# Kernel optimization log

Measured on AMD Instinct MI355X. Metric: run time of the kernel, lower is better.

Reference implementation:

```python
import jax, jax.numpy as jnp
import numpy as np

B, S, D, H, SKG = 4, 1024, 1024, 16, 256
HD = D // H  # head dim = 64


def setup_inputs() -> dict:
    key = jax.random.key(0)
    ks = jax.random.split(key, 8)
    std = 0.02
    return {
        "x": jax.random.normal(ks[0], (B, S, D), dtype=jnp.float32),
        "pred_kg": jax.random.normal(ks[1], (B, SKG, D), dtype=jnp.float32),
        "Wc": jax.random.normal(ks[2], (D, 3 * D), dtype=jnp.float32) * std,  # c_attn weight
        "bc": jnp.zeros((3 * D,), dtype=jnp.float32),
        "Wk": jax.random.normal(ks[3], (D, 2 * D), dtype=jnp.float32) * std,  # k_attn weight
        "bk": jnp.zeros((2 * D,), dtype=jnp.float32),
        "Wp": jax.random.normal(ks[4], (D, D), dtype=jnp.float32) * std,     # c_proj weight (shared)
        "bp": jnp.zeros((D,), dtype=jnp.float32),
    }


def _split_heads(t):  # [B, T, D] -> [B, H, T, HD]
    Bb, T, _ = t.shape
    return t.reshape(Bb, T, H, HD).transpose(0, 2, 1, 3)


def _merge_heads(t):  # [B, H, T, HD] -> [B, T, D]
    Bb, _, T, _ = t.shape
    return t.transpose(0, 2, 1, 3).reshape(Bb, T, D)


def reference(x, pred_kg, Wc, bc, Wk, bk, Wp, bp):
    # ---- self-attention branch (GPT-2 style, explicit causal bias blend) ----
    qkv = x @ Wc + bc                       # Conv1D: [B,S,3D]
    q, k, v = jnp.split(qkv, 3, axis=-1)
    q = _split_heads(q)                     # [B,H,S,HD]
    k = _split_heads(k)
    v = _split_heads(v)

    inv_sqrt_d = 1.0 / jnp.sqrt(jnp.float32(HD))
    w = jnp.einsum("bhqd,bhkd->bhqk", q, k) * inv_sqrt_d  # [B,H,S,S]
    causal = jnp.tril(jnp.ones((S, S), dtype=w.dtype))    # bias buffer slice b
    # faithful to: w = w * b - 10000.0 * (1 - b)
    w = w * causal - 10000.0 * (1.0 - causal)
    w = jax.nn.softmax(w, axis=-1)
    a = jnp.einsum("bhqk,bhkd->bhqd", w, v)
    a = _merge_heads(a) @ Wp + bp           # c_proj; resid dropout is identity in eval

    # ---- KG cross-attention branch (shares query and c_proj) ----
    kkv = pred_kg @ Wk + bk                 # [B,SKG,2D]
    kk, kv = jnp.split(kkv, 2, axis=-1)
    kk = _split_heads(kk)                   # [B,H,SKG,HD]
    kv = _split_heads(kv)
    w2 = jnp.einsum("bhqd,bhkd->bhqk", q, kk) * inv_sqrt_d  # [B,H,S,SKG]
    w2 = jax.nn.softmax(w2, axis=-1)
    ka = jnp.einsum("bhqk,bhkd->bhqd", w2, kv)
    ka = _merge_heads(ka) @ Wp + bp

    # concat the two branch outputs along the sequence axis: [B, S+SKG, D]
    return jnp.concatenate([a, ka], axis=1)
```

## Files before the change

### kernel.cpp

```cpp
#include <hip/hip_runtime.h>
#include <hip/hip_bf16.h>

typedef __bf16 bf16_t;
typedef bf16_t bf16x8 __attribute__((ext_vector_type(8)));
typedef bf16_t bf16x4 __attribute__((ext_vector_type(4)));
typedef float f32x4 __attribute__((ext_vector_type(4)));
typedef float f32x16 __attribute__((ext_vector_type(16)));

#define EXP2C 0.1803368867f
#define FEXP2(x) __builtin_amdgcn_exp2f(x)

__device__ __forceinline__ void gload16(const void* g, void* l) {
  __builtin_amdgcn_global_load_lds(
      (const __attribute__((address_space(1))) void*)g,
      (__attribute__((address_space(3))) void*)l, 16, 0, 0);
}

__device__ __forceinline__ unsigned pkbf(float lo, float hi) {
  unsigned short a = __builtin_bit_cast(unsigned short, (bf16_t)lo);
  unsigned short b = __builtin_bit_cast(unsigned short, (bf16_t)hi);
  return (unsigned)a | ((unsigned)b << 16);
}

__device__ __forceinline__ void plswap(unsigned& a, unsigned& b) {
#if __has_builtin(__builtin_amdgcn_permlane32_swap)
  auto r = __builtin_amdgcn_permlane32_swap(a, b, false, false);
  a = r[0]; b = r[1];
#else
  asm("v_permlane32_swap_b32 %0, %1" : "+v"(a), "+v"(b));
#endif
}
__device__ __forceinline__ float xmax32(float x) {
  unsigned a = __builtin_bit_cast(unsigned, x), b = a;
  plswap(a, b);
  return fmaxf(__builtin_bit_cast(float, a), __builtin_bit_cast(float, b));
}
__device__ __forceinline__ float xsum32(float x) {
  unsigned a = __builtin_bit_cast(unsigned, x), b = a;
  plswap(a, b);
  return __builtin_bit_cast(float, a) + __builtin_bit_cast(float, b);
}

__global__ __launch_bounds__(256) void prep_kernel(
    const float* __restrict__ x, bf16_t* __restrict__ xb,
    const float* __restrict__ pkg, bf16_t* __restrict__ pkb,
    const float* __restrict__ Wc, bf16_t* __restrict__ Wct,
    const float* __restrict__ Wk, bf16_t* __restrict__ Wkt,
    const float* __restrict__ Wp, bf16_t* __restrict__ Wpt) {
  __shared__ float tile[32][33];
  const int bid = blockIdx.x, tid = threadIdx.x;
  if (bid < 5120) {
    int i = bid * 256 + tid;
    const float* src; bf16_t* dst;
    if (i < 1048576) { src = x; dst = xb; }
    else { i -= 1048576; src = pkg; dst = pkb; }
    float4 v = reinterpret_cast<const float4*>(src)[i];
    bf16x4 o = { (bf16_t)v.x, (bf16_t)v.y, (bf16_t)v.z, (bf16_t)v.w };
    reinterpret_cast<bf16x4*>(dst)[i] = o;
    return;
  }
  int r = bid - 5120;
  int xx = r % 192, ky = r / 192;
  const float* W; bf16_t* T; int N;
  if (xx < 96) { W = Wc; T = Wct; N = 3072; }
  else if (xx < 160) { W = Wk; T = Wkt; N = 2048; xx -= 96; }
  else { W = Wp; T = Wpt; N = 1024; xx -= 160; }
  const int K = 1024;
  int tx = tid & 31, ty = tid >> 5;
  int n0 = xx * 32, k0 = ky * 32;
#pragma unroll
  for (int i = 0; i < 4; ++i)
    tile[ty + i * 8][tx] = W[(size_t)(k0 + ty + i * 8) * N + n0 + tx];
  __syncthreads();
#pragma unroll
  for (int i = 0; i < 4; ++i)
    T[(size_t)(n0 + ty + i * 8) * K + k0 + tx] = (bf16_t)tile[tx][ty + i * 8];
}

__global__ __launch_bounds__(256) void pack2_kernel(
    const bf16_t* __restrict__ src0, bf16_t* __restrict__ kd0, bf16_t* __restrict__ vd0,
    const bf16_t* __restrict__ src1, bf16_t* __restrict__ kd1, bf16_t* __restrict__ vd1) {
  __shared__ bf16_t vt[32][72];
  const int tid = threadIdx.x;
  int x = blockIdx.x;
  const int bh = blockIdx.y;
  const bf16_t* src; bf16_t *kd, *vd; int R, stride, kcol, vcol, NT, t;
  if (x < 32) { src = src0; kd = kd0; vd = vd0; R = 1024; stride = 3072; kcol = 1024; vcol = 2048; NT = 32; t = x; }
  else        { src = src1; kd = kd1; vd = vd1; R = 256;  stride = 2048; kcol = 0;    vcol = 1024; NT = 8;  t = x - 32; }
  const int b = bh >> 4, h = bh & 15;
  const size_t srow = (size_t)b * R + t * 32;
  const size_t obase = ((size_t)bh * NT + t) * 2048;
  {
    int r = tid >> 3, c = tid & 7;
    bf16x8 d = *(const bf16x8*)&src[(srow + r) * stride + vcol + h * 64 + c * 8];
    *(bf16x8*)&vt[r][c * 8] = d;
  }
  {
    int ks = tid >> 6, l = tid & 63;
    int hi8 = (l >> 5) * 8;
    bf16x8 d = *(const bf16x8*)&src[(srow + (l & 31)) * stride + kcol + h * 64 + ks * 16 + hi8];
    *(bf16x8*)&kd[obase + ks * 512 + l * 8] = d;
  }
  __syncthreads();
  {
    int dd = tid >> 6, l = tid & 63;
    int mb = dd >> 1, ks = dd & 1;
    int hd = mb * 32 + (l & 31);
    int kvr = ks * 16 + (l >> 5) * 8;
    bf16x8 o;
#pragma unroll
    for (int j = 0; j < 8; ++j) o[j] = vt[kvr + j][hd];
    *(bf16x8*)&vd[obase + dd * 512 + l * 8] = o;
  }
}

#define GBAR() __builtin_amdgcn_s_barrier()
#define LGKM0() asm volatile("s_waitcnt lgkmcnt(0)" ::: "memory")

__device__ __forceinline__ void gemm256_body(
    char* smem, const bf16_t* __restrict__ A, const bf16_t* __restrict__ Bt,
    const float* __restrict__ bias, bf16_t* __restrict__ Cout,
    int N, int K, int bx, int by) {
  const int tid = threadIdx.x;
  const int l = tid & 63, w = tid >> 6;
  const int lr = l & 15, lg = l >> 4;
  const int m0 = by * 256, n0 = bx * 256;
  const int wr = (w >> 2) * 128, wc = (w & 3) * 64;
  const int hA = w >> 2, hB = (w >> 1) & 1;

  const int sr = tid >> 3;
  const int scb = ((tid & 7) * 16) ^ ((sr & 7) << 4);
  const bf16_t* Ab = A + (size_t)m0 * K + (scb >> 1);
  const bf16_t* Bb = Bt + (size_t)n0 * K + (scb >> 1);
  const int nk = K >> 6;
  const int xr = (lr & 7) << 4;

  auto STAGE_A = [&](int t, int h) {
    const bf16_t* g = Ab + (size_t)(h * 128 + sr) * K + t * 64;
    char* d = smem + ((size_t)(t & 1) * 2 + h) * 16384 + tid * 16;
    gload16(g, d);
    gload16(g + (size_t)64 * K, d + 8192);
  };
  auto STAGE_B = [&](int t, int h) {
    const bf16_t* g = Bb + (size_t)(h * 128 + sr) * K + t * 64;
    char* d = smem + 65536 + ((size_t)(t & 1) * 2 + h) * 16384 + tid * 16;
    gload16(g, d);
    gload16(g + (size_t)64 * K, d + 8192);
  };

  f32x4 acc[8][4] = {};
  bf16x8 af[4][2], bf[2][2][2];

  STAGE_A(0, 0); STAGE_A(0, 1); STAGE_B(0, 0); STAGE_B(0, 1);
  asm volatile("s_waitcnt vmcnt(0)" ::: "memory");
  GBAR();

  for (int t = 0; t < nk; ++t) {
    const char* pA = smem + ((size_t)(t & 1) * 2 + hA) * 16384;
    const char* pB = smem + 65536 + ((size_t)(t & 1) * 2 + hB) * 16384;
    auto LDA = [&](int mf, int ks) {
      return *(const bf16x8*)(pA + (mf * 16 + lr) * 128 + ((ks * 64 + lg * 16) ^ xr));
    };
    auto LDB = [&](int nf, int ks) {
      return *(const bf16x8*)(pB + ((w & 1) * 64 + nf * 16 + lr) * 128 + ((ks * 64 + lg * 16) ^ xr));
    };
#pragma unroll
    for (int mf = 0; mf < 4; ++mf) { af[mf][0] = LDA(mf, 0); af[mf][1] = LDA(mf, 1); }
#pragma unroll
    for (int nf = 0; nf < 2; ++nf) { bf[0][nf][0] = LDB(nf, 0); bf[0][nf][1] = LDB(nf, 1); }
    if (t + 1 < nk) { STAGE_A(t + 1, 0); STAGE_B(t + 1, 0); }
    GBAR(); LGKM0();
    __builtin_amdgcn_s_setprio(1);
#pragma unroll
    for (int mf = 0; mf < 4; ++mf)
#pragma unroll
      for (int nf = 0; nf < 2; ++nf) {
        acc[mf][nf] = __builtin_amdgcn_mfma_f32_16x16x32_bf16(af[mf][0], bf[0][nf][0], acc[mf][nf], 0, 0, 0);
        acc[mf][nf] = __builtin_amdgcn_mfma_f32_16x16x32_bf16(af[mf][1], bf[0][nf][1], acc[mf][nf], 0, 0, 0);
      }
    __builtin_amdgcn_s_setprio(0);
    GBAR();
#pragma unroll
    for (int nf = 0; nf < 2; ++nf) { bf[1][nf][0] = LDB(2 + nf, 0); bf[1][nf][1] = LDB(2 + nf, 1); }
    if (t + 1 < nk) { STAGE_A(t + 1, 1); STAGE_B(t + 1, 1); }
    GBAR(); LGKM0();
    __builtin_amdgcn_s_setprio(1);
#pragma unroll
    for (int mf = 0; mf < 4; ++mf)
#pragma unroll
      for (int nf = 0; nf < 2; ++nf) {
        acc[mf][2 + nf] = __builtin_amdgcn_mfma_f32_16x16x32_bf16(af[mf][0], bf[1][nf][0], acc[mf][2 + nf], 0, 0, 0);
        acc[mf][2 + nf] = __builtin_amdgcn_mfma_f32_16x16x32_bf16(af[mf][1], bf[1][nf][1], acc[mf][2 + nf], 0, 0, 0);
      }
    __builtin_amdgcn_s_setprio(0);
    GBAR();
#pragma unroll
    for (int mf = 0; mf < 4; ++mf) { af[mf][0] = LDA(4 + mf, 0); af[mf][1] = LDA(4 + mf, 1); }
    GBAR(); LGKM0();
    __builtin_amdgcn_s_setprio(1);
#pragma unroll
    for (int mf = 0; mf < 4; ++mf)
#pragma unroll
      for (int nf = 0; nf < 2; ++nf) {
        acc[4 + mf][nf] = __builtin_amdgcn_mfma_f32_16x16x32_bf16(af[mf][0], bf[0][nf][0], acc[4 + mf][nf], 0, 0, 0);
        acc[4 + mf][nf] = __builtin_amdgcn_mfma_f32_16x16x32_bf16(af[mf][1], bf[0][nf][1], acc[4 + mf][nf], 0, 0, 0);
      }
    __builtin_amdgcn_s_setprio(0);
    GBAR();
    __builtin_amdgcn_s_setprio(1);
#pragma unroll
    for (int mf = 0; mf < 4; ++mf)
#pragma unroll
      for (int nf = 0; nf < 2; ++nf) {
        acc[4 + mf][2 + nf] = __builtin_amdgcn_mfma_f32_16x16x32_bf16(af[mf][0], bf[1][nf][0], acc[4 + mf][2 + nf], 0, 0, 0);
        acc[4 + mf][2 + nf] = __builtin_amdgcn_mfma_f32_16x16x32_bf16(af[mf][1], bf[1][nf][1], acc[4 + mf][2 + nf], 0, 0, 0);
      }
    __builtin_amdgcn_s_setprio(0);
    asm volatile("s_waitcnt vmcnt(0)" ::: "memory");
    GBAR();
  }

#pragma unroll
  for (int mf = 0; mf < 8; ++mf) {
#pragma unroll
    for (int nf = 0; nf < 4; ++nf) {
      int col = n0 + wc + nf * 16 + lr;
      float bb = bias[col];
      int rowb = m0 + wr + mf * 16 + lg * 4;
#pragma unroll
      for (int r = 0; r < 4; ++r) {
        float v = acc[mf][nf][r] + bb;
        ((bf16_t*)Cout)[(size_t)(rowb + r) * N + col] = (bf16_t)v;
      }
    }
  }
}

__global__ __launch_bounds__(512, 1) void gemm2_kernel(
    const bf16_t* __restrict__ A0, const bf16_t* __restrict__ B0,
    const float* __restrict__ bi0, bf16_t* __restrict__ C0,
    const bf16_t* __restrict__ A1, const bf16_t* __restrict__ B1,
    const float* __restrict__ bi1, bf16_t* __restrict__ C1) {
  extern __shared__ char smem[];
  int bid = blockIdx.x;
  int wg = (bid & 7) * 28 + (bid >> 3);
  if (wg < 192)
    gemm256_body(smem, A0, B0, bi0, C0, 3072, 1024, wg % 12, wg / 12);
  else {
    int r = wg - 192;
    gemm256_body(smem, A1, B1, bi1, C1, 2048, 1024, r % 8, r / 8);
  }
}

#define MFMA2(mi, ni)                                                         \
  acc[mi][ni] = __builtin_amdgcn_mfma_f32_16x16x32_bf16(af[(mi) & 1][0], bf[ni][0], acc[mi][ni], 0, 0, 0); \
  acc[mi][ni] = __builtin_amdgcn_mfma_f32_16x16x32_bf16(af[(mi) & 1][1], bf[ni][1], acc[mi][ni], 0, 0, 0);
#define MFMA8(qm, qn)                                                         \
  MFMA2(2 * (qm) + 0, 2 * (qn) + 0) MFMA2(2 * (qm) + 0, 2 * (qn) + 1)         \
  MFMA2(2 * (qm) + 1, 2 * (qn) + 0) MFMA2(2 * (qm) + 1, 2 * (qn) + 1)

template <int OUTF32>
__device__ __forceinline__ void gemm8_body(
    char* smem, const bf16_t* __restrict__ A, const bf16_t* __restrict__ Bt,
    const float* __restrict__ bias, void* __restrict__ Cout,
    int N, int K, int bx, int by) {
  const int tid = threadIdx.x;
  const int l = tid & 63, w = tid >> 6;
  const int lr = l & 15, lg = l >> 4;
  const int m0 = by * 256, n0 = bx * 128;
  const int wr = (w >> 1) * 64, wc = (w & 1) * 64;

  const int sr = tid >> 3;
  const int scb = ((tid & 7) * 16) ^ ((sr & 7) << 4);
  const bf16_t* Ab = A + (size_t)m0 * K + (scb >> 1);
  const bf16_t* Bb = Bt + (size_t)n0 * K + (scb >> 1);
  const int nk = K >> 6;

  const int hA = w >> 2;
  const int rA = ((w >> 1) & 1) * 64 + lr;
  const int rB = wc + lr;
  const int xr = (lr & 7) << 4;

  auto STAGE_A = [&](int t, int h) {
    const bf16_t* g = Ab + (size_t)(h * 128 + sr) * K + t * 64;
    char* d = smem + ((size_t)(t & 1) * 2 + h) * 16384 + tid * 16;
    gload16(g, d);
    gload16(g + (size_t)64 * K, d + 8192);
  };
  auto STAGE_B = [&](int t) {
    const bf16_t* g = Bb + (size_t)sr * K + t * 64;
    char* d = smem + 65536 + (size_t)(t & 1) * 16384 + tid * 16;
    gload16(g, d);
    gload16(g + (size_t)64 * K, d + 8192);
  };

  f32x4 acc[4][4] = {};
  bf16x8 af[2][2], bf[4][2];

  STAGE_A(0, 0); STAGE_A(0, 1); STAGE_B(0); STAGE_B(1); STAGE_A(1, 0);
  asm volatile("s_waitcnt vmcnt(4)" ::: "memory");
  GBAR();

  for (int t = 0; t < nk; ++t) {
    const char* pA = smem + ((size_t)(t & 1) * 2 + hA) * 16384;
    const char* pB = smem + 65536 + (size_t)(t & 1) * 16384;
    auto LDA = [&](int mf, int ks) {
      return *(const bf16x8*)(pA + (rA + mf * 16) * 128 + ((ks * 64 + lg * 16) ^ xr));
    };
    auto LDB = [&](int nf, int ks) {
      return *(const bf16x8*)(pB + (rB + nf * 16) * 128 + ((ks * 64 + lg * 16) ^ xr));
    };
    af[0][0] = LDA(0, 0); af[0][1] = LDA(0, 1);
    af[1][0] = LDA(1, 0); af[1][1] = LDA(1, 1);
    bf[0][0] = LDB(0, 0); bf[0][1] = LDB(0, 1);
    bf[1][0] = LDB(1, 0); bf[1][1] = LDB(1, 1);
    if (t + 1 < nk) STAGE_A(t + 1, 1);
    GBAR(); LGKM0();
    __builtin_amdgcn_s_setprio(1);
    MFMA8(0, 0)
    __builtin_amdgcn_s_setprio(0);
    GBAR();
    bf[2][0] = LDB(2, 0); bf[2][1] = LDB(2, 1);
    bf[3][0] = LDB(3, 0); bf[3][1] = LDB(3, 1);
    GBAR(); LGKM0();
    __builtin_amdgcn_s_setprio(1);
    MFMA8(0, 1)
    __builtin_amdgcn_s_setprio(0);
    GBAR();
    af[0][0] = LDA(2, 0); af[0][1] = LDA(2, 1);
    af[1][0] = LDA(3, 0); af[1][1] = LDA(3, 1);
    if (t + 2 < nk) STAGE_B(t + 2);
    GBAR(); LGKM0();
    __builtin_amdgcn_s_setprio(1);
    MFMA8(1, 0)
    __builtin_amdgcn_s_setprio(0);
    GBAR();
    if (t + 2 < nk) STAGE_A(t + 2, 0);
    GBAR();
    __builtin_amdgcn_s_setprio(1);
    MFMA8(1, 1)
    __builtin_amdgcn_s_setprio(0);
    if (t + 2 < nk)      asm volatile("s_waitcnt vmcnt(4)" ::: "memory");
    else if (t + 1 < nk) asm volatile("s_waitcnt vmcnt(0)" ::: "memory");
    GBAR();
  }

#pragma unroll
  for (int mf = 0; mf < 4; ++mf) {
#pragma unroll
    for (int nf = 0; nf < 4; ++nf) {
      int col = n0 + wc + nf * 16 + lr;
      float bb = bias[col];
      int rowb = m0 + wr + mf * 16 + lg * 4;
#pragma unroll
      for (int r = 0; r < 4; ++r) {
        float v = acc[mf][nf][r] + bb;
        if constexpr (OUTF32)
          ((float*)Cout)[(size_t)(rowb + r) * N + col] = v;
        else
          ((bf16_t*)Cout)[(size_t)(rowb + r) * N + col] = (bf16_t)v;
      }
    }
  }
}

__global__ __launch_bounds__(512, 1) void gemm_proj_kernel(
    const bf16_t* __restrict__ A, const bf16_t* __restrict__ Bt,
    const float* __restrict__ bias, float* __restrict__ Cout) {
  extern __shared__ char smem[];
  int bid = blockIdx.x;
  int wg = (bid & 7) * 32 + (bid >> 3);
  gemm8_body<1>(smem, A, Bt, bias, Cout, 1024, 1024, wg % 8, wg / 8);
}

#define STAGE64(bf, it)                                                       \
  {                                                                           \
    gload16(kba + (size_t)(it) * 4096 + tid * 8, &sKV[bf][tid * 16]);         \
    gload16(kba + (size_t)(it) * 4096 + 2048 + tid * 8, &sKV[bf][4096 + tid * 16]); \
    gload16(vba + (size_t)(it) * 4096 + tid * 8, &sKV[bf][8192 + tid * 16]);  \
    gload16(vba + (size_t)(it) * 4096 + 2048 + tid * 8, &sKV[bf][12288 + tid * 16]); \
  }
#define QKT(sub)                                                              \
  {                                                                           \
    _Pragma("unroll") for (int c = 0; c < 4; ++c)                             \
        kf[c] = *(const bf16x8*)&sKV[buf][(sub) * 4096 + c * 1024 + l * 16];  \
    sa = (f32x16){};                                                          \
    __builtin_amdgcn_s_setprio(1);                                            \
    _Pragma("unroll") for (int ks = 0; ks < 4; ++ks)                          \
        sa = __builtin_amdgcn_mfma_f32_32x32x16_bf16(kf[ks], qf[ks], sa, 0, 0, 0); \
    __builtin_amdgcn_s_setprio(0);                                            \
  }
#define SMPV(sub, tcur)                                                       \
  {                                                                           \
    _Pragma("unroll") for (int c = 0; c < 4; ++c)                             \
        vf[c] = *(const bf16x8*)&sKV[buf][8192 + (sub) * 4096 + c * 1024 + l * 16]; \
    float sv[16];                                                             \
    const bool mt = is_self && ((tcur) == qw);                                \
    _Pragma("unroll") for (int r = 0; r < 16; ++r) {                          \
      float v = sa[r];                                                        \
      if (mt) {                                                               \
        int kvr = (r & 3) + 8 * (r >> 2) + kv4;                               \
        v = (kvr > ql) ? -1e30f : v;                                          \
      }                                                                       \
      sv[r] = v;                                                              \
    }                                                                         \
    float tm = fmaxf(                                                         \
        fmaxf(fmaxf(fmaxf(sv[0], sv[1]), fmaxf(sv[2], sv[3])),                \
              fmaxf(fmaxf(sv[4], sv[5]), fmaxf(sv[6], sv[7]))),               \
        fmaxf(fmaxf(fmaxf(sv[8], sv[9]), fmaxf(sv[10], sv[11])),              \
              fmaxf(fmaxf(sv[12], sv[13]), fmaxf(sv[14], sv[15]))));          \
    tm = xmax32(tm);                                                          \
    if (!__all(tm <= mcur + 64.f)) {                                          \
      float mn = fmaxf(mcur, tm);                                             \
      float sc = FEXP2((mcur - mn) * EXP2C);                                  \
      mcur = mn;                                                              \
      lcur *= sc;                                                             \
      _Pragma("unroll") for (int mb = 0; mb < 2; ++mb)                        \
          _Pragma("unroll") for (int r = 0; r < 16; ++r) oacc[mb][r] *= sc;   \
    }                                                                         \
    const float hm = mcur * EXP2C;                                            \
    float pf[16];                                                             \
    _Pragma("unroll") for (int r = 0; r < 16; ++r)                            \
        pf[r] = FEXP2(__builtin_fmaf(sv[r], EXP2C, -hm));                     \
    float ps = (((pf[0] + pf[1]) + (pf[2] + pf[3])) +                         \
                ((pf[4] + pf[5]) + (pf[6] + pf[7]))) +                        \
               (((pf[8] + pf[9]) + (pf[10] + pf[11])) +                       \
                ((pf[12] + pf[13]) + (pf[14] + pf[15])));                     \
    ps = xsum32(ps);                                                          \
    lcur += ps;                                                               \
    unsigned o01 = pkbf(pf[0], pf[1]), o23 = pkbf(pf[2], pf[3]);              \
    unsigned o45 = pkbf(pf[4], pf[5]), o67 = pkbf(pf[6], pf[7]);              \
    unsigned o89 = pkbf(pf[8], pf[9]), o1011 = pkbf(pf[10], pf[11]);          \
    unsigned o1213 = pkbf(pf[12], pf[13]), o1415 = pkbf(pf[14], pf[15]);      \
    plswap(o01, o45); plswap(o23, o67);                                       \
    plswap(o89, o1213); plswap(o1011, o1415);                                 \
    uint4 w0 = { o01, o23, o45, o67 };                                        \
    uint4 w1 = { o89, o1011, o1213, o1415 };                                  \
    bf16x8 pb0 = __builtin_bit_cast(bf16x8, w0);                              \
    bf16x8 pb1 = __builtin_bit_cast(bf16x8, w1);                              \
    __builtin_amdgcn_s_setprio(1);                                            \
    oacc[0] = __builtin_amdgcn_mfma_f32_32x32x16_bf16(vf[0], pb0, oacc[0], 0, 0, 0); \
    oacc[0] = __builtin_amdgcn_mfma_f32_32x32x16_bf16(vf[1], pb1, oacc[0], 0, 0, 0); \
    oacc[1] = __builtin_amdgcn_mfma_f32_32x32x16_bf16(vf[2], pb0, oacc[1], 0, 0, 0); \
    oacc[1] = __builtin_amdgcn_mfma_f32_32x32x16_bf16(vf[3], pb1, oacc[1], 0, 0, 0); \
    __builtin_amdgcn_s_setprio(0);                                            \
  }

__global__ __launch_bounds__(256) void attn_kernel(
    const bf16_t* __restrict__ qkv,
    const bf16_t* __restrict__ kfs, const bf16_t* __restrict__ vfs,
    const bf16_t* __restrict__ kfc, const bf16_t* __restrict__ vfc,
    bf16_t* __restrict__ obuf) {
  __shared__ __align__(16) char sKV[2][16384];

  const int tid = threadIdx.x;
  const int w = tid >> 6, l = tid & 63;
  const int ql = l & 31;
  const bool uhi = l >= 32;
  const int kv4 = uhi ? 4 : 0;
  const int hi8 = uhi ? 8 : 0;

  const int bid = blockIdx.x;
  const bool is_self = bid < 512;
  int qb, bh, nt32;
  if (is_self) {
    qb = 7 - (bid >> 6);
    bh = bid & 63;
    nt32 = qb * 4 + 4;
  } else {
    int cb = bid - 512;
    qb = cb >> 6;
    bh = cb & 63;
    nt32 = 8;
  }
  const int qw = qb * 4 + w;
  const int b = bh >> 4, h = bh & 15;
  const int hcol = h * 64;
  const int q0 = qw * 32;
  const int tlim = is_self ? qw : (nt32 - 1);
  const int nit = nt32 >> 1;

  const bf16_t* kba; const bf16_t* vba; int ooff;
  if (is_self) {
    kba = kfs + (size_t)bh * 32 * 2048; vba = vfs + (size_t)bh * 32 * 2048; ooff = 0;
  } else {
    kba = kfc + (size_t)bh * 8 * 2048;  vba = vfc + (size_t)bh * 8 * 2048;  ooff = 1024;
  }

  const bf16_t* qrow = qkv + (size_t)(b * 1024 + q0 + ql) * 3072 + hcol + hi8;
  bf16x8 qf[4];
#pragma unroll
  for (int ks = 0; ks < 4; ++ks) qf[ks] = *(const bf16x8*)(qrow + ks * 16);

  float mcur = -1e30f, lcur = 0.f;
  f32x16 oacc[2] = {};
  f32x16 sa;
  bf16x8 kf[4], vf[4];

  STAGE64(0, 0);
  __syncthreads();
  int buf = 0;
  for (int it = 0; it < nit; ++it) {
    if (it + 1 < nit) STAGE64(buf ^ 1, it + 1);
    const int t0 = 2 * it, t1 = 2 * it + 1;
    if (t0 <= tlim) {
      QKT(0);
      SMPV(0, t0);
    }
    if (t1 <= tlim) {
      QKT(1);
      SMPV(1, t1);
    }
    __syncthreads();
    buf ^= 1;
  }

  const float rl = 1.0f / lcur;
  char* swp = &sKV[0][0] + w * 4096;
#pragma unroll
  for (int mb = 0; mb < 2; ++mb)
#pragma unroll
    for (int r2 = 0; r2 < 8; ++r2) {
      float lo = oacc[mb][2 * r2] * rl;
      float hiv = oacc[mb][2 * r2 + 1] * rl;
      int hdb = (r2 & 1) * 2 + 8 * (r2 >> 1) + kv4 + mb * 32;
      int off = (ql * 128 + hdb * 2) ^ ((ql & 7) << 4);
      *(unsigned*)(swp + off) = pkbf(lo, hiv);
    }
  __syncthreads();
  const int orow = b * 2048 + ooff + q0;
#pragma unroll
  for (int it = 0; it < 4; ++it) {
    int idx = it * 64 + l;
    int q = idx >> 3, ch = idx & 7;
    int off = (q * 128 + ch * 16) ^ ((q & 7) << 4);
    uint4 d = *(uint4*)(swp + off);
    *(uint4*)&obuf[(size_t)(orow + q) * 1024 + hcol + ch * 8] = d;
  }
}

extern "C" void kernel_launch(void* const* d_in, const int* in_sizes, int n_in,
                              void* d_out, int out_size, void* d_ws, size_t ws_size,
                              hipStream_t stream) {
  (void)in_sizes; (void)n_in; (void)out_size; (void)ws_size;
  const float* x   = (const float*)d_in[0];
  const float* pkg = (const float*)d_in[1];
  const float* Wc  = (const float*)d_in[2];
  const float* bc  = (const float*)d_in[3];
  const float* Wk  = (const float*)d_in[4];
  const float* bk  = (const float*)d_in[5];
  const float* Wp  = (const float*)d_in[6];
  const float* bp  = (const float*)d_in[7];
  float* out = (float*)d_out;

  char* ws = (char*)d_ws;
  const size_t MB = 1u << 20;
  bf16_t* xb   = (bf16_t*)(ws + 0 * MB);
  bf16_t* pkb  = (bf16_t*)(ws + 8 * MB);
  bf16_t* Wct  = (bf16_t*)(ws + 10 * MB);
  bf16_t* Wkt  = (bf16_t*)(ws + 16 * MB);
  bf16_t* Wpt  = (bf16_t*)(ws + 20 * MB);
  bf16_t* kkvb = (bf16_t*)(ws + 22 * MB);
  bf16_t* abuf = (bf16_t*)(ws + 26 * MB);
  bf16_t* vfs  = (bf16_t*)(ws + 0 * MB);
  bf16_t* kfc  = (bf16_t*)(ws + 8 * MB);
  bf16_t* vfc  = (bf16_t*)(ws + 10 * MB);
  bf16_t* qkvb = (bf16_t*)d_out;
  bf16_t* kfs  = (bf16_t*)((char*)d_out + 24 * MB);

  prep_kernel<<<11264, 256, 0, stream>>>(x, xb, pkg, pkb, Wc, Wct, Wk, Wkt, Wp, Wpt);
  gemm2_kernel<<<224, 512, 131072, stream>>>(xb, Wct, bc, qkvb, pkb, Wkt, bk, kkvb);
  pack2_kernel<<<dim3(40, 64), 256, 0, stream>>>(qkvb, kfs, vfs, kkvb, kfc, vfc);
  attn_kernel<<<1024, 256, 0, stream>>>(qkvb, kfs, vfs, kfc, vfc, abuf);
  gemm_proj_kernel<<<256, 512, 98304, stream>>>(abuf, Wpt, bp, out);
}
```

Before: 110.7 us.

## Fuse K/V fragment packing into QKV GEMM epilogue, drop pack kernel

```diff
diff --git a/kernel.cpp b/kernel.cpp
--- a/kernel.cpp
+++ b/kernel.cpp
@@ -77,50 +77,14 @@
     T[(size_t)(n0 + ty + i * 8) * K + k0 + tx] = (bf16_t)tile[tx][ty + i * 8];
 }
 
-__global__ __launch_bounds__(256) void pack2_kernel(
-    const bf16_t* __restrict__ src0, bf16_t* __restrict__ kd0, bf16_t* __restrict__ vd0,
-    const bf16_t* __restrict__ src1, bf16_t* __restrict__ kd1, bf16_t* __restrict__ vd1) {
-  __shared__ bf16_t vt[32][72];
-  const int tid = threadIdx.x;
-  int x = blockIdx.x;
-  const int bh = blockIdx.y;
-  const bf16_t* src; bf16_t *kd, *vd; int R, stride, kcol, vcol, NT, t;
-  if (x < 32) { src = src0; kd = kd0; vd = vd0; R = 1024; stride = 3072; kcol = 1024; vcol = 2048; NT = 32; t = x; }
-  else        { src = src1; kd = kd1; vd = vd1; R = 256;  stride = 2048; kcol = 0;    vcol = 1024; NT = 8;  t = x - 32; }
-  const int b = bh >> 4, h = bh & 15;
-  const size_t srow = (size_t)b * R + t * 32;
-  const size_t obase = ((size_t)bh * NT + t) * 2048;
-  {
-    int r = tid >> 3, c = tid & 7;
-    bf16x8 d = *(const bf16x8*)&src[(srow + r) * stride + vcol + h * 64 + c * 8];
-    *(bf16x8*)&vt[r][c * 8] = d;
-  }
-  {
-    int ks = tid >> 6, l = tid & 63;
-    int hi8 = (l >> 5) * 8;
-    bf16x8 d = *(const bf16x8*)&src[(srow + (l & 31)) * stride + kcol + h * 64 + ks * 16 + hi8];
-    *(bf16x8*)&kd[obase + ks * 512 + l * 8] = d;
-  }
-  __syncthreads();
-  {
-    int dd = tid >> 6, l = tid & 63;
-    int mb = dd >> 1, ks = dd & 1;
-    int hd = mb * 32 + (l & 31);
-    int kvr = ks * 16 + (l >> 5) * 8;
-    bf16x8 o;
-#pragma unroll
-    for (int j = 0; j < 8; ++j) o[j] = vt[kvr + j][hd];
-    *(bf16x8*)&vd[obase + dd * 512 + l * 8] = o;
-  }
-}
-
 #define GBAR() __builtin_amdgcn_s_barrier()
 #define LGKM0() asm volatile("s_waitcnt lgkmcnt(0)" ::: "memory")
 
 __device__ __forceinline__ void gemm256_body(
     char* smem, const bf16_t* __restrict__ A, const bf16_t* __restrict__ Bt,
-    const float* __restrict__ bias, bf16_t* __restrict__ Cout,
-    int N, int K, int bx, int by) {
+    const float* __restrict__ bias, bf16_t* __restrict__ Cout, int N,
+    int K, int bx, int by, int mode, bf16_t* __restrict__ fdst,
+    int NT, int bfb, int h0, int t0) {
   const int tid = threadIdx.x;
   const int l = tid & 63, w = tid >> 6;
   const int lr = l & 15, lg = l >> 4;
@@ -220,18 +184,71 @@
     GBAR();
   }
 
+  if (mode == 0) {
+#pragma unroll
+    for (int mf = 0; mf < 8; ++mf) {
+#pragma unroll
+      for (int nf = 0; nf < 4; ++nf) {
+        int col = n0 + wc + nf * 16 + lr;
+        float bb = bias[col];
+        int rowb = m0 + wr + mf * 16 + lg * 4;
+#pragma unroll
+        for (int r = 0; r < 4; ++r) {
+          float v = acc[mf][nf][r] + bb;
+          Cout[(size_t)(rowb + r) * N + col] = (bf16_t)v;
+        }
+      }
+    }
+    return;
+  }
+
 #pragma unroll
   for (int mf = 0; mf < 8; ++mf) {
 #pragma unroll
     for (int nf = 0; nf < 4; ++nf) {
-      int col = n0 + wc + nf * 16 + lr;
-      float bb = bias[col];
-      int rowb = m0 + wr + mf * 16 + lg * 4;
+      int lcol = wc + nf * 16 + lr;
+      float bb = bias[n0 + lcol];
+      int rowb = wr + mf * 16 + lg * 4;
 #pragma unroll
       for (int r = 0; r < 4; ++r) {
-        float v = acc[mf][nf][r] + bb;
-        ((bf16_t*)Cout)[(size_t)(rowb + r) * N + col] = (bf16_t)v;
-      }
+        int lrow = rowb + r;
+        *(bf16_t*)(smem + lrow * 512 + ((lcol * 2) ^ ((lrow & 7) << 4))) =
+            (bf16_t)(acc[mf][nf][r] + bb);
+      }
+    }
+  }
+  __syncthreads();
+  if (mode == 1) {
+#pragma unroll
+    for (int i = 0; i < 16; ++i) {
+      int g = i * 512 + tid;
+      int sub = g >> 8, c = g & 255;
+      int ks = c >> 6, l2 = c & 63;
+      int tt = sub >> 2, hc = sub & 3;
+      int lrow = tt * 32 + (l2 & 31);
+      int lcol = hc * 64 + ks * 16 + ((l2 >> 5) * 8);
+      uint4 d = *(uint4*)(smem + lrow * 512 + ((lcol * 2) ^ ((lrow & 7) << 4)));
+      size_t obase = ((size_t)(bfb + h0 + hc) * NT + (t0 + tt)) * 2048;
+      *(uint4*)&fdst[obase + ks * 512 + (size_t)l2 * 8] = d;
+    }
+  } else {
+#pragma unroll
+    for (int i = 0; i < 16; ++i) {
+      int g = i * 512 + tid;
+      int sub = g >> 8, c = g & 255;
+      int dd = c >> 6, l2 = c & 63;
+      int mb = dd >> 1, ks = dd & 1;
+      int tt = sub >> 2, hc = sub & 3;
+      int kvr = ks * 16 + ((l2 >> 5) * 8);
+      int lcolv = hc * 64 + mb * 32 + (l2 & 31);
+      bf16_t tmp[8];
+#pragma unroll
+      for (int j = 0; j < 8; ++j) {
+        int lrow = tt * 32 + kvr + j;
+        tmp[j] = *(bf16_t*)(smem + lrow * 512 + ((lcolv * 2) ^ ((lrow & 7) << 4)));
+      }
+      size_t obase = ((size_t)(bfb + h0 + hc) * NT + (t0 + tt)) * 2048;
+      *(bf16x8*)&fdst[obase + dd * 512 + (size_t)l2 * 8] = *(bf16x8*)tmp;
     }
   }
 }
@@ -240,15 +257,28 @@
     const bf16_t* __restrict__ A0, const bf16_t* __restrict__ B0,
     const float* __restrict__ bi0, bf16_t* __restrict__ C0,
     const bf16_t* __restrict__ A1, const bf16_t* __restrict__ B1,
-    const float* __restrict__ bi1, bf16_t* __restrict__ C1) {
+    const float* __restrict__ bi1,
+    bf16_t* __restrict__ kfs, bf16_t* __restrict__ vfs,
+    bf16_t* __restrict__ kfc, bf16_t* __restrict__ vfc) {
   extern __shared__ char smem[];
   int bid = blockIdx.x;
   int wg = (bid & 7) * 28 + (bid >> 3);
-  if (wg < 192)
-    gemm256_body(smem, A0, B0, bi0, C0, 3072, 1024, wg % 12, wg / 12);
-  else {
+  if (wg < 192) {
+    int bx = wg % 12, by = wg / 12;
+    int b = by >> 2, t0 = (by & 3) * 8;
+    if (bx < 4)
+      gemm256_body(smem, A0, B0, bi0, C0, 3072, 1024, bx, by, 0, nullptr, 0, 0, 0, 0);
+    else if (bx < 8)
+      gemm256_body(smem, A0, B0, bi0, nullptr, 3072, 1024, bx, by, 1, kfs, 32, b * 16, (bx - 4) * 4, t0);
+    else
+      gemm256_body(smem, A0, B0, bi0, nullptr, 3072, 1024, bx, by, 2, vfs, 32, b * 16, (bx - 8) * 4, t0);
+  } else {
     int r = wg - 192;
-    gemm256_body(smem, A1, B1, bi1, C1, 2048, 1024, r % 8, r / 8);
+    int bx = r % 8, by = r / 8;
+    if (bx < 4)
+      gemm256_body(smem, A1, B1, bi1, nullptr, 2048, 1024, bx, by, 1, kfc, 8, by * 16, bx * 4, 0);
+    else
+      gemm256_body(smem, A1, B1, bi1, nullptr, 2048, 1024, bx, by, 2, vfc, 8, by * 16, (bx - 4) * 4, 0);
   }
 }
 
@@ -259,10 +289,9 @@
   MFMA2(2 * (qm) + 0, 2 * (qn) + 0) MFMA2(2 * (qm) + 0, 2 * (qn) + 1)         \
   MFMA2(2 * (qm) + 1, 2 * (qn) + 0) MFMA2(2 * (qm) + 1, 2 * (qn) + 1)
 
-template <int OUTF32>
 __device__ __forceinline__ void gemm8_body(
     char* smem, const bf16_t* __restrict__ A, const bf16_t* __restrict__ Bt,
-    const float* __restrict__ bias, void* __restrict__ Cout,
+    const float* __restrict__ bias, float* __restrict__ Cout,
     int N, int K, int bx, int by) {
   const int tid = threadIdx.x;
   const int l = tid & 63, w = tid >> 6;
@@ -355,10 +384,7 @@
 #pragma unroll
       for (int r = 0; r < 4; ++r) {
         float v = acc[mf][nf][r] + bb;
-        if constexpr (OUTF32)
-          ((float*)Cout)[(size_t)(rowb + r) * N + col] = v;
-        else
-          ((bf16_t*)Cout)[(size_t)(rowb + r) * N + col] = (bf16_t)v;
+        Cout[(size_t)(rowb + r) * N + col] = v;
       }
     }
   }
@@ -370,7 +396,7 @@
   extern __shared__ char smem[];
   int bid = blockIdx.x;
   int wg = (bid & 7) * 32 + (bid >> 3);
-  gemm8_body<1>(smem, A, Bt, bias, Cout, 1024, 1024, wg % 8, wg / 8);
+  gemm8_body(smem, A, Bt, bias, Cout, 1024, 1024, wg % 8, wg / 8);
 }
 
 #define STAGE64(bf, it)                                                       \
@@ -560,17 +586,16 @@
   bf16_t* Wct  = (bf16_t*)(ws + 10 * MB);
   bf16_t* Wkt  = (bf16_t*)(ws + 16 * MB);
   bf16_t* Wpt  = (bf16_t*)(ws + 20 * MB);
-  bf16_t* kkvb = (bf16_t*)(ws + 22 * MB);
-  bf16_t* abuf = (bf16_t*)(ws + 26 * MB);
-  bf16_t* vfs  = (bf16_t*)(ws + 0 * MB);
-  bf16_t* kfc  = (bf16_t*)(ws + 8 * MB);
-  bf16_t* vfc  = (bf16_t*)(ws + 10 * MB);
+  bf16_t* vfs  = (bf16_t*)(ws + 22 * MB);
+  bf16_t* kfc  = (bf16_t*)(ws + 30 * MB);
+  bf16_t* vfc  = (bf16_t*)(ws + 32 * MB);
+  bf16_t* abuf = (bf16_t*)(ws + 34 * MB);
   bf16_t* qkvb = (bf16_t*)d_out;
   bf16_t* kfs  = (bf16_t*)((char*)d_out + 24 * MB);
 
   prep_kernel<<<11264, 256, 0, stream>>>(x, xb, pkg, pkb, Wc, Wct, Wk, Wkt, Wp, Wpt);
-  gemm2_kernel<<<224, 512, 131072, stream>>>(xb, Wct, bc, qkvb, pkb, Wkt, bk, kkvb);
-  pack2_kernel<<<dim3(40, 64), 256, 0, stream>>>(qkvb, kfs, vfs, kkvb, kfc, vfc);
+  gemm2_kernel<<<224, 512, 131072, stream>>>(xb, Wct, bc, qkvb, pkb, Wkt, bk,
+                                             kfs, vfs, kfc, vfc);
   attn_kernel<<<1024, 256, 0, stream>>>(qkvb, kfs, vfs, kfc, vfc, abuf);
   gemm_proj_kernel<<<256, 512, 98304, stream>>>(abuf, Wpt, bp, out);
 }
```

New measurement: 101.8 us (median of 2 runs). 1.09x faster.
